# Kernel optimization log

Hardware: AMD Instinct MI355X
Metric: run time of the kernel (lower is better)

Reference implementation:

```python
import jax, jax.numpy as jnp
import numpy as np

IN_DIM = 4096
OUT_DIM = 4096
BLOCK = 256
RANK = 16
B_IN = IN_DIM // BLOCK   # 16
B_OUT = OUT_DIM // BLOCK # 16


def setup_inputs() -> dict:
    key = jax.random.key(0)
    k1, k2, k3, k4, k5 = jax.random.split(key, 5)
    x = jax.random.normal(k1, (2, 1024, IN_DIM), dtype=jnp.float32)
    # S ~ U[0, 2)
    S = jax.random.uniform(k2, (B_OUT, B_IN, RANK), dtype=jnp.float32, minval=0.0, maxval=2.0)
    std = np.sqrt(0.02).astype(np.float32)
    U = jax.random.normal(k3, (B_OUT, RANK, BLOCK), dtype=jnp.float32) * std
    Vt = jax.random.normal(k4, (B_IN, BLOCK, RANK), dtype=jnp.float32) * std
    # kaiming_uniform_ on a (1, out_dim) tensor with default a=sqrt(5): bound = 1/sqrt(fan_in) = 1/sqrt(out_dim)
    bound = float(1.0 / np.sqrt(OUT_DIM))
    bias = jax.random.uniform(k5, (OUT_DIM,), dtype=jnp.float32, minval=-bound, maxval=bound)
    return {"x": x, "S": S, "U": U, "Vt": Vt, "bias": bias}


def reference(x, S, U, Vt, bias):
    # Faithful to Blast.forward: it reconstructs the dense weight by running
    # forward2 on an identity matrix (which ALSO adds bias to every row of W),
    # then computes addmm(bias, x, W).
    # Block (i_in, i_out) of W0 = Vt[i_in] @ diag(S[i_out, i_in]) @ U[i_out].
    W0 = jnp.einsum('ipr,oir,orq->ipoq', Vt, S, U).reshape(IN_DIM, OUT_DIM)
    W = W0 + bias[None, :]  # identity-trick: forward2(I) adds bias to each of the in_dim rows
    out = x @ W + bias      # [B, S, out_dim]
    return out
```

## Files before the change

### kernel.cpp

```cpp
#include <hip/hip_runtime.h>

#define IN_DIM  4096
#define OUT_DIM 4096
#define RANK    16
#define NBLK    16
#define KDIM    256

typedef __attribute__((ext_vector_type(8))) __bf16 bf16x8;
typedef __attribute__((ext_vector_type(4))) __bf16 bf16x4;
typedef __attribute__((ext_vector_type(4))) float  f32x4;


__device__ __forceinline__ void split_bf16(float v, __bf16& h, __bf16& l) {
    h = (__bf16)v;
    l = (__bf16)(v - (float)h);
}

__global__ __launch_bounds__(256) void build_packs(const float* __restrict__ S,
                                                   const float* __restrict__ U,
                                                   const float* __restrict__ Vt,
                                                   bf16x8* __restrict__ Bhi,
                                                   bf16x8* __restrict__ Blo,
                                                   bf16x8* __restrict__ Vhi,
                                                   bf16x8* __restrict__ Vlo) {
    const int blk = blockIdx.x;
    if (blk < 512) {
        int t  = blk * 256 + threadIdx.x;
        int c  = t & 15;
        int ko = (t >> 4) & 31;
        int nt = t >> 9;
        int o  = nt >> 4;
        int i  = ko >> 1;
        int q  = ((nt & 15) << 4) | c;
        int r0 = (ko & 1) << 3;
        const float* Sp = S + ((o * NBLK + i) * RANK + r0);
        const float* Up = U + (size_t)o * RANK * 256 + q;
        bf16x8 hi, lo;
#pragma unroll
        for (int j = 0; j < 8; ++j) {
            float w = Sp[j] * Up[(size_t)(r0 + j) * 256];
            __bf16 h, l;
            split_bf16(w, h, l);
            hi[j] = h; lo[j] = l;
        }
        Bhi[t] = hi;
        Blo[t] = lo;
    } else {
        int t  = (blk - 512) * 256 + threadIdx.x;
        int c  = t & 15;
        int p0 = (t >> 4) << 3;
        int i  = t >> 9;
        int pbase = (p0 & 255);
        const float* vp = Vt + ((size_t)(i * 256 + pbase)) * RANK + c;
        bf16x8 hi, lo;
#pragma unroll
        for (int j = 0; j < 8; ++j) {
            float w = vp[(size_t)j * RANK];
            __bf16 h, l;
            split_bf16(w, h, l);
            hi[j] = h; lo[j] = l;
        }
        Vhi[t] = hi;
        Vlo[t] = lo;
    }
}

__global__ __launch_bounds__(256) void factor_mfma(const float* __restrict__ x,
                                                   const bf16x8* __restrict__ Vhi,
                                                   const bf16x8* __restrict__ Vlo,
                                                   bf16x4* __restrict__ Ahi4,
                                                   bf16x4* __restrict__ Alo4,
                                                   float* __restrict__ rowsum_p,
                                                   int M) {
    const int tid = threadIdx.x;
    const int l   = tid & 63;
    const int w   = tid >> 6;
    const int job = blockIdx.x * 4 + w;
    const int i   = job & 15;
    const int mt  = job >> 4;
    const int row = l & 15;
    const int qt  = l >> 4;

    const float* xp = x + (size_t)(mt * 16 + row) * IN_DIM + i * 256 + qt * 8;

    f32x4 acc = {0.f, 0.f, 0.f, 0.f};
    float rs = 0.f;
#pragma unroll
    for (int ks = 0; ks < 8; ++ks) {
        float4 a = *reinterpret_cast<const float4*>(xp + ks * 32);
        float4 b = *reinterpret_cast<const float4*>(xp + ks * 32 + 4);
        rs += (a.x + a.y) + (a.z + a.w) + (b.x + b.y) + (b.z + b.w);
        float vv[8] = {a.x, a.y, a.z, a.w, b.x, b.y, b.z, b.w};
        bf16x8 xh, xl;
#pragma unroll
        for (int jj = 0; jj < 8; ++jj) {
            __bf16 h, lo_;
            split_bf16(vv[jj], h, lo_);
            xh[jj] = h; xl[jj] = lo_;
        }
        size_t vidx = (size_t)((i * 8 + ks) * 4 + qt) * 16 + row;
        bf16x8 vh = Vhi[vidx];
        bf16x8 vl = Vlo[vidx];
        acc = __builtin_amdgcn_mfma_f32_16x16x32_bf16(vh, xh, acc, 0, 0, 0);
        acc = __builtin_amdgcn_mfma_f32_16x16x32_bf16(vh, xl, acc, 0, 0, 0);
        acc = __builtin_amdgcn_mfma_f32_16x16x32_bf16(vl, xh, acc, 0, 0, 0);
    }

    rs += __shfl_xor(rs, 16, 64);
    rs += __shfl_xor(rs, 32, 64);
    if (l < 16)
        rowsum_p[(size_t)i * M + mt * 16 + l] = rs;

    bf16x4 hi, lo;
#pragma unroll
    for (int reg = 0; reg < 4; ++reg) {
        __bf16 h, lo_;
        split_bf16(acc[reg], h, lo_);
        hi[reg] = h; lo[reg] = lo_;
    }
    size_t o4 = ((size_t)(mt * 32 + i * 2 + (l >> 5)) * 16 + row) * 2 + ((l >> 4) & 1);
    Ahi4[o4] = hi;
    Alo4[o4] = lo;
}

__global__ __launch_bounds__(256, 3) void apply_mfma(const bf16x8* __restrict__ Ahi,
                                                     const bf16x8* __restrict__ Alo,
                                                     const bf16x8* __restrict__ Bhi,
                                                     const bf16x8* __restrict__ Blo,
                                                     const float* __restrict__ rowsum_p,
                                                     const float* __restrict__ bias,
                                                     float* __restrict__ out, int M) {
    __shared__ bf16x8 smem[2][1536];
    __shared__ float rstot_s[64];

    const int nb  = blockIdx.x;
    const int q   = gridDim.x >> 3;
    const int lg  = (nb & 7) * q + (nb >> 3);
    const int mr  = lg & 31;
    const int nc  = lg >> 5;
    const int m0  = mr * 64, n0 = nc * 128;
    const int mtb0 = m0 >> 4;
    const int ntb0 = n0 >> 4;

    const int tid = threadIdx.x;
    const int l   = tid & 63;
    const int w   = __builtin_amdgcn_readfirstlane(tid >> 6);
    const int wm  = w & 1, wn = w >> 1;
    const int kq  = l >> 4, c = l & 15;

#define STAGE(s_, buf_)                                                              \
    {                                                                                \
        _Pragma("unroll")                                                            \
        for (int j = 0; j < 6; ++j) {                                                \
            const int sl = w * 6 + j;                                                \
            const bf16x8* gbase;                                                     \
            if (sl < 8) {                                                            \
                gbase = ((sl >> 2) ? Alo : Ahi)                                      \
                      + ((size_t)(mtb0 + (sl & 3)) * 32 + 4 * (s_)) * 16;            \
            } else {                                                                 \
                const int b = sl - 8;                                                \
                gbase = ((b >> 3) ? Blo : Bhi)                                       \
                      + ((size_t)(ntb0 + (b & 7)) * 32 + 4 * (s_)) * 16;             \
            }                                                                        \
            __builtin_amdgcn_global_load_lds(                                        \
                (const __attribute__((address_space(1))) unsigned*)(gbase + l),      \
                (__attribute__((address_space(3))) unsigned*)&smem[buf_][sl * 64],   \
                16, 0, 0);                                                           \
        }                                                                            \
    }

    f32x4 acc[2][4];
#pragma unroll
    for (int f = 0; f < 2; ++f)
#pragma unroll
        for (int nf = 0; nf < 4; ++nf) acc[f][nf] = f32x4{0.f, 0.f, 0.f, 0.f};

    STAGE(0, 0);
    if (tid < 64) {
        float ssum = 1.0f;
#pragma unroll
        for (int i = 0; i < NBLK; ++i) ssum += rowsum_p[(size_t)i * M + m0 + tid];
        rstot_s[tid] = ssum;
    }
    __syncthreads();

    for (int s = 0; s < 8; ++s) {
        if (s < 7) STAGE(s + 1, (s + 1) & 1);
        const bf16x8* sb = smem[s & 1];
        bf16x8 ah[2], al[2];
#pragma unroll
        for (int f = 0; f < 2; ++f) {
            ah[f] = sb[(wm * 2 + f) * 64 + l];
            al[f] = sb[(4 + wm * 2 + f) * 64 + l];
        }
#pragma unroll
        for (int nf = 0; nf < 4; ++nf) {
            bf16x8 bh = sb[512 + (wn * 4 + nf) * 64 + l];
            bf16x8 bl = sb[1024 + (wn * 4 + nf) * 64 + l];
#pragma unroll
            for (int f = 0; f < 2; ++f) {
                acc[f][nf] = __builtin_amdgcn_mfma_f32_16x16x32_bf16(ah[f], bh, acc[f][nf], 0, 0, 0);
                acc[f][nf] = __builtin_amdgcn_mfma_f32_16x16x32_bf16(ah[f], bl, acc[f][nf], 0, 0, 0);
                acc[f][nf] = __builtin_amdgcn_mfma_f32_16x16x32_bf16(al[f], bh, acc[f][nf], 0, 0, 0);
            }
        }
        __syncthreads();
    }
#undef STAGE

#pragma unroll
    for (int f = 0; f < 2; ++f) {
        const int rloc = wm * 32 + f * 16 + kq * 4;
        const int rowb = m0 + rloc;
        float rsv[4];
#pragma unroll
        for (int reg = 0; reg < 4; ++reg) rsv[reg] = rstot_s[rloc + reg];
#pragma unroll
        for (int nf = 0; nf < 4; ++nf) {
            const int n = n0 + wn * 64 + nf * 16 + c;
            const float bv = bias[n];
#pragma unroll
            for (int reg = 0; reg < 4; ++reg)
                out[(size_t)(rowb + reg) * OUT_DIM + n] = acc[f][nf][reg] + rsv[reg] * bv;
        }
    }
}

extern "C" void kernel_launch(void* const* d_in, const int* in_sizes, int n_in,
                              void* d_out, int out_size, void* d_ws, size_t ws_size,
                              hipStream_t stream) {
    const float* x    = (const float*)d_in[0];
    const float* S    = (const float*)d_in[1];
    const float* U    = (const float*)d_in[2];
    const float* Vt   = (const float*)d_in[3];
    const float* bias = (const float*)d_in[4];
    float* out = (float*)d_out;
    const int M = in_sizes[0] / IN_DIM;

    char* ws = (char*)d_ws;
    bf16x8* Bhi     = (bf16x8*)ws;
    bf16x8* Blo     = (bf16x8*)(ws + (2u << 20));
    bf16x8* Ahi     = (bf16x8*)(ws + (4u << 20));
    bf16x8* Alo     = (bf16x8*)(ws + (5u << 20));
    bf16x8* Vhi     = (bf16x8*)(ws + (6u << 20));
    bf16x8* Vlo     = (bf16x8*)(ws + (6u << 20) + (128u << 10));
    float* rowsum_p = (float*)(ws + (6u << 20) + (256u << 10));

    build_packs<<<544, 256, 0, stream>>>(S, U, Vt, Bhi, Blo, Vhi, Vlo);
    factor_mfma<<<M / 4, 256, 0, stream>>>(x, Vhi, Vlo,
                                           (bf16x4*)Ahi, (bf16x4*)Alo, rowsum_p, M);
    apply_mfma<<<(M / 64) * (OUT_DIM / 128), 256, 0, stream>>>(
        Ahi, Alo, Bhi, Blo, rowsum_p, bias, out, M);
}
```

Before: 116.9 us.

## Drop low-order B split and enlarge apply tile to 128x128

Removes the bf16 low-part of the combined S*U factor, so the apply GEMM issues two MFMAs per fragment pair instead of three and stages only hi B. With the LDS freed, each block covers 128 rows instead of 64, which halves the grid and doubles reuse of the B tile. This reduces accuracy of the B operand to plain bf16, and raising the accumulator count to 64 floats per thread may cost occupancy under launch_bounds(256,3).

```diff
diff --git a/kernel.cpp b/kernel.cpp
--- a/kernel.cpp
+++ b/kernel.cpp
@@ -20,7 +20,6 @@
                                                    const float* __restrict__ U,
                                                    const float* __restrict__ Vt,
                                                    bf16x8* __restrict__ Bhi,
-                                                   bf16x8* __restrict__ Blo,
                                                    bf16x8* __restrict__ Vhi,
                                                    bf16x8* __restrict__ Vlo) {
     const int blk = blockIdx.x;
@@ -35,16 +34,13 @@
         int r0 = (ko & 1) << 3;
         const float* Sp = S + ((o * NBLK + i) * RANK + r0);
         const float* Up = U + (size_t)o * RANK * 256 + q;
-        bf16x8 hi, lo;
+        bf16x8 hi;
 #pragma unroll
         for (int j = 0; j < 8; ++j) {
             float w = Sp[j] * Up[(size_t)(r0 + j) * 256];
-            __bf16 h, l;
-            split_bf16(w, h, l);
-            hi[j] = h; lo[j] = l;
+            hi[j] = (__bf16)w;
         }
         Bhi[t] = hi;
-        Blo[t] = lo;
     } else {
         int t  = (blk - 512) * 256 + threadIdx.x;
         int c  = t & 15;
@@ -126,19 +122,18 @@
 __global__ __launch_bounds__(256, 3) void apply_mfma(const bf16x8* __restrict__ Ahi,
                                                      const bf16x8* __restrict__ Alo,
                                                      const bf16x8* __restrict__ Bhi,
-                                                     const bf16x8* __restrict__ Blo,
                                                      const float* __restrict__ rowsum_p,
                                                      const float* __restrict__ bias,
                                                      float* __restrict__ out, int M) {
     __shared__ bf16x8 smem[2][1536];
-    __shared__ float rstot_s[64];
+    __shared__ float rstot_s[128];
 
     const int nb  = blockIdx.x;
     const int q   = gridDim.x >> 3;
     const int lg  = (nb & 7) * q + (nb >> 3);
-    const int mr  = lg & 31;
-    const int nc  = lg >> 5;
-    const int m0  = mr * 64, n0 = nc * 128;
+    const int mr  = lg & 15;
+    const int nc  = lg >> 4;
+    const int m0  = mr * 128, n0 = nc * 128;
     const int mtb0 = m0 >> 4;
     const int ntb0 = n0 >> 4;
 
@@ -154,14 +149,12 @@
         for (int j = 0; j < 6; ++j) {                                                \
             const int sl = w * 6 + j;                                                \
             const bf16x8* gbase;                                                     \
-            if (sl < 8) {                                                            \
-                gbase = ((sl >> 2) ? Alo : Ahi)                                      \
-                      + ((size_t)(mtb0 + (sl & 3)) * 32 + 4 * (s_)) * 16;            \
-            } else {                                                                 \
-                const int b = sl - 8;                                                \
-                gbase = ((b >> 3) ? Blo : Bhi)                                       \
-                      + ((size_t)(ntb0 + (b & 7)) * 32 + 4 * (s_)) * 16;             \
-            }                                                                        \
+            if (sl < 8)                                                              \
+                gbase = Ahi + ((size_t)((mtb0 + sl) * 32 + 4 * (s_)) * 16);          \
+            else if (sl < 16)                                                        \
+                gbase = Alo + ((size_t)((mtb0 + sl - 8) * 32 + 4 * (s_)) * 16);      \
+            else                                                                     \
+                gbase = Bhi + ((size_t)((ntb0 + sl - 16) * 32 + 4 * (s_)) * 16);     \
             __builtin_amdgcn_global_load_lds(                                        \
                 (const __attribute__((address_space(1))) unsigned*)(gbase + l),      \
                 (__attribute__((address_space(3))) unsigned*)&smem[buf_][sl * 64],   \
@@ -169,14 +162,14 @@
         }                                                                            \
     }
 
-    f32x4 acc[2][4];
-#pragma unroll
-    for (int f = 0; f < 2; ++f)
+    f32x4 acc[4][4];
+#pragma unroll
+    for (int f = 0; f < 4; ++f)
 #pragma unroll
         for (int nf = 0; nf < 4; ++nf) acc[f][nf] = f32x4{0.f, 0.f, 0.f, 0.f};
 
     STAGE(0, 0);
-    if (tid < 64) {
+    if (tid < 128) {
         float ssum = 1.0f;
 #pragma unroll
         for (int i = 0; i < NBLK; ++i) ssum += rowsum_p[(size_t)i * M + m0 + tid];
@@ -187,20 +180,18 @@
     for (int s = 0; s < 8; ++s) {
         if (s < 7) STAGE(s + 1, (s + 1) & 1);
         const bf16x8* sb = smem[s & 1];
-        bf16x8 ah[2], al[2];
-#pragma unroll
-        for (int f = 0; f < 2; ++f) {
-            ah[f] = sb[(wm * 2 + f) * 64 + l];
-            al[f] = sb[(4 + wm * 2 + f) * 64 + l];
+        bf16x8 ah[4], al[4];
+#pragma unroll
+        for (int f = 0; f < 4; ++f) {
+            ah[f] = sb[(wm * 4 + f) * 64 + l];
+            al[f] = sb[512 + (wm * 4 + f) * 64 + l];
         }
 #pragma unroll
         for (int nf = 0; nf < 4; ++nf) {
-            bf16x8 bh = sb[512 + (wn * 4 + nf) * 64 + l];
-            bf16x8 bl = sb[1024 + (wn * 4 + nf) * 64 + l];
-#pragma unroll
-            for (int f = 0; f < 2; ++f) {
+            bf16x8 bh = sb[1024 + (wn * 4 + nf) * 64 + l];
+#pragma unroll
+            for (int f = 0; f < 4; ++f) {
                 acc[f][nf] = __builtin_amdgcn_mfma_f32_16x16x32_bf16(ah[f], bh, acc[f][nf], 0, 0, 0);
-                acc[f][nf] = __builtin_amdgcn_mfma_f32_16x16x32_bf16(ah[f], bl, acc[f][nf], 0, 0, 0);
                 acc[f][nf] = __builtin_amdgcn_mfma_f32_16x16x32_bf16(al[f], bh, acc[f][nf], 0, 0, 0);
             }
         }
@@ -209,8 +200,8 @@
 #undef STAGE
 
 #pragma unroll
-    for (int f = 0; f < 2; ++f) {
-        const int rloc = wm * 32 + f * 16 + kq * 4;
+    for (int f = 0; f < 4; ++f) {
+        const int rloc = wm * 64 + f * 16 + kq * 4;
         const int rowb = m0 + rloc;
         float rsv[4];
 #pragma unroll
@@ -239,16 +230,15 @@
 
     char* ws = (char*)d_ws;
     bf16x8* Bhi     = (bf16x8*)ws;
-    bf16x8* Blo     = (bf16x8*)(ws + (2u << 20));
-    bf16x8* Ahi     = (bf16x8*)(ws + (4u << 20));
-    bf16x8* Alo     = (bf16x8*)(ws + (5u << 20));
-    bf16x8* Vhi     = (bf16x8*)(ws + (6u << 20));
-    bf16x8* Vlo     = (bf16x8*)(ws + (6u << 20) + (128u << 10));
-    float* rowsum_p = (float*)(ws + (6u << 20) + (256u << 10));
-
-    build_packs<<<544, 256, 0, stream>>>(S, U, Vt, Bhi, Blo, Vhi, Vlo);
+    bf16x8* Ahi     = (bf16x8*)(ws + (2u << 20));
+    bf16x8* Alo     = (bf16x8*)(ws + (3u << 20));
+    bf16x8* Vhi     = (bf16x8*)(ws + (4u << 20));
+    bf16x8* Vlo     = (bf16x8*)(ws + (4u << 20) + (128u << 10));
+    float* rowsum_p = (float*)(ws + (4u << 20) + (256u << 10));
+
+    build_packs<<<544, 256, 0, stream>>>(S, U, Vt, Bhi, Vhi, Vlo);
     factor_mfma<<<M / 4, 256, 0, stream>>>(x, Vhi, Vlo,
                                            (bf16x4*)Ahi, (bf16x4*)Alo, rowsum_p, M);
-    apply_mfma<<<(M / 64) * (OUT_DIM / 128), 256, 0, stream>>>(
-        Ahi, Alo, Bhi, Blo, rowsum_p, bias, out, M);
-}
+    apply_mfma<<<(M / 128) * (OUT_DIM / 128), 256, 0, stream>>>(
+        Ahi, Alo, Bhi, rowsum_p, bias, out, M);
+}
```

New measurement: 108.9 us. 6.8% less time.
